# Kernel optimization log

Measured on AMD Instinct MI355X. Metric: run time of the kernel, lower is better.

Reference implementation:

```python
import jax, jax.numpy as jnp
import numpy as np

B, S, H, D = 2, 4096, 32, 128
R = 2            # num_reflectors
BASE = 10000.0   # rope base
EPS = 1e-6


def setup_inputs() -> dict:
    key = jax.random.key(0)
    k1, k2, k3 = jax.random.split(key, 3)
    q = jax.random.normal(k1, (B, S, H, D), jnp.float32)
    k = jax.random.normal(k2, (B, S, H, D), jnp.float32)
    pos = jnp.arange(S, dtype=jnp.float32)
    reflectors = jax.random.normal(k3, (H, R, D), jnp.float32)
    return {"q": q, "k": k, "pos": pos, "reflectors": reflectors}


def _apply_householder(x, reflectors, eps):
    # x: [B,S,H,D]; reflectors: [H,R,D]. Apply chain of per-head reflections
    # H = prod_r (I - 2 v_r v_r^T / (||v_r||^2 + eps)).
    n_refl = reflectors.shape[1]
    for r in range(n_refl):  # small fixed loop over reflectors
        v = reflectors[:, r, :]                      # [H,D]
        vf = v.astype(jnp.float32)
        sq = jnp.sum(vf * vf, axis=-1) + eps         # [H], fp32 accumulation
        dot = jnp.einsum('bshd,hd->bsh', x.astype(jnp.float32), vf)  # [B,S,H]
        coef = (2.0 * dot / sq).astype(x.dtype)      # [B,S,H]
        x = x - coef[..., None] * v                  # rank-1 update per head
    return x


def _rope(x, pos, base):
    # Block-diagonal 2x2 rotations on adjacent pairs (rope_ndim=2).
    d = x.shape[-1]
    d2 = d // 2
    inv_freq = base ** (-(jnp.arange(d2, dtype=jnp.float32) * 2.0) / d)  # [d2]
    ang = pos[:, None] * inv_freq                     # [S,d2]
    cos = jnp.cos(ang)[None, :, None, :]              # [1,S,1,d2]
    sin = jnp.sin(ang)[None, :, None, :]
    xr = x.reshape(*x.shape[:-1], d2, 2)              # [B,S,H,d2,2]
    x0, x1 = xr[..., 0], xr[..., 1]
    out = jnp.stack([x0 * cos - x1 * sin, x0 * sin + x1 * cos], axis=-1)
    return out.reshape(x.shape)


def reference(q, k, pos, reflectors):
    qh = _apply_householder(q, reflectors, EPS)
    kh = _apply_householder(k, reflectors, EPS)
    return _rope(qh, pos, BASE), _rope(kh, pos, BASE)
```

## Files before the change

kernel.cpp:

```cpp
#include <hip/hip_runtime.h>
#include <math.h>

#define BB 2
#define SS 4096
#define HH 32
#define DD 128
#define EPS_C 1e-6f
#define C_LOG (-0.20762050593046015f)

__device__ __forceinline__ float half_reduce(float v) {
    v += __shfl_xor(v, 1, 64);
    v += __shfl_xor(v, 2, 64);
    v += __shfl_xor(v, 4, 64);
    v += __shfl_xor(v, 8, 64);
    v += __shfl_xor(v, 16, 64);
    return v;
}

__global__ __launch_bounds__(256)
void hh_rope_kernel(const float* __restrict__ q, const float* __restrict__ k,
                    const float* __restrict__ pos, const float* __restrict__ refl,
                    float* __restrict__ oq, float* __restrict__ ok)
{
    const int lane   = threadIdx.x & 63;
    const int wid    = blockIdx.x * (blockDim.x >> 6) + (threadIdx.x >> 6);
    const int nW     = gridDim.x * (blockDim.x >> 6);
    const int hp     = wid & 15;
    const int slice  = wid >> 4;
    const int nSlice = nW >> 4;
    const int half   = lane >> 5;
    const int j      = lane & 31;
    const int h      = hp * 2 + half;

    const float4 v0 = ((const float4*)(refl + (size_t)(h * 2 + 0) * DD))[j];
    const float4 v1 = ((const float4*)(refl + (size_t)(h * 2 + 1) * DD))[j];
    const float rs0 = 2.0f / (half_reduce(v0.x*v0.x + v0.y*v0.y + v0.z*v0.z + v0.w*v0.w) + EPS_C);
    const float rs1 = 2.0f / (half_reduce(v1.x*v1.x + v1.y*v1.y + v1.z*v1.z + v1.w*v1.w) + EPS_C);

    const float if0 = exp2f((float)(2 * j)     * C_LOG);
    const float if1 = exp2f((float)(2 * j + 1) * C_LOG);

    for (int bs = slice; bs < BB * SS; bs += nSlice) {
        const float p = pos[bs & (SS - 1)];
        const size_t off = ((size_t)bs * HH + h) * DD + 4 * (size_t)j;

        float4 xq = *(const float4*)(q + off);
        float4 xk = *(const float4*)(k + off);

        float dq = half_reduce(xq.x*v0.x + xq.y*v0.y + xq.z*v0.z + xq.w*v0.w) * rs0;
        float dk = half_reduce(xk.x*v0.x + xk.y*v0.y + xk.z*v0.z + xk.w*v0.w) * rs0;
        xq.x -= dq * v0.x; xq.y -= dq * v0.y; xq.z -= dq * v0.z; xq.w -= dq * v0.w;
        xk.x -= dk * v0.x; xk.y -= dk * v0.y; xk.z -= dk * v0.z; xk.w -= dk * v0.w;

        dq = half_reduce(xq.x*v1.x + xq.y*v1.y + xq.z*v1.z + xq.w*v1.w) * rs1;
        dk = half_reduce(xk.x*v1.x + xk.y*v1.y + xk.z*v1.z + xk.w*v1.w) * rs1;
        xq.x -= dq * v1.x; xq.y -= dq * v1.y; xq.z -= dq * v1.z; xq.w -= dq * v1.w;
        xk.x -= dk * v1.x; xk.y -= dk * v1.y; xk.z -= dk * v1.z; xk.w -= dk * v1.w;

        float s0, c0, s1, c1;
        __sincosf(p * if0, &s0, &c0);
        __sincosf(p * if1, &s1, &c1);

        float4 rq, rk;
        rq.x = xq.x * c0 - xq.y * s0;  rq.y = xq.x * s0 + xq.y * c0;
        rq.z = xq.z * c1 - xq.w * s1;  rq.w = xq.z * s1 + xq.w * c1;
        rk.x = xk.x * c0 - xk.y * s0;  rk.y = xk.x * s0 + xk.y * c0;
        rk.z = xk.z * c1 - xk.w * s1;  rk.w = xk.z * s1 + xk.w * c1;

        *(float4*)(oq + off) = rq;
        *(float4*)(ok + off) = rk;
    }
}

extern "C" void kernel_launch(void* const* d_in, const int* in_sizes, int n_in,
                              void* d_out, int out_size, void* d_ws, size_t ws_size,
                              hipStream_t stream) {
    const float* q    = (const float*)d_in[0];
    const float* k    = (const float*)d_in[1];
    const float* pos  = (const float*)d_in[2];
    const float* refl = (const float*)d_in[3];

    float* oq = (float*)d_out;
    float* ok = oq + (size_t)BB * SS * HH * DD;

    hh_rope_kernel<<<dim3(2048), dim3(256), 0, stream>>>(q, k, pos, refl, oq, ok);
}
```

Measured before the change: 438.7 us.

## Fuse both Householder reflections algebraically, process two rows per iteration, nontemporal IO

```diff
diff --git a/kernel.cpp b/kernel.cpp
--- a/kernel.cpp
+++ b/kernel.cpp
@@ -8,67 +8,95 @@
 #define EPS_C 1e-6f
 #define C_LOG (-0.20762050593046015f)
 
-__device__ __forceinline__ float half_reduce(float v) {
-    v += __shfl_xor(v, 1, 64);
-    v += __shfl_xor(v, 2, 64);
-    v += __shfl_xor(v, 4, 64);
-    v += __shfl_xor(v, 8, 64);
-    v += __shfl_xor(v, 16, 64);
+typedef float vf4 __attribute__((ext_vector_type(4)));
+
+__device__ __forceinline__ float hsum32(float v) {
+    v += __int_as_float(__builtin_amdgcn_ds_swizzle(__float_as_int(v), 0x041F));
+    v += __int_as_float(__builtin_amdgcn_ds_swizzle(__float_as_int(v), 0x081F));
+    v += __int_as_float(__builtin_amdgcn_ds_swizzle(__float_as_int(v), 0x101F));
+    v += __int_as_float(__builtin_amdgcn_ds_swizzle(__float_as_int(v), 0x201F));
+    v += __int_as_float(__builtin_amdgcn_ds_swizzle(__float_as_int(v), 0x401F));
     return v;
 }
 
-__global__ __launch_bounds__(256)
+__device__ __forceinline__ float dot4(vf4 a, vf4 b) {
+    return a.x * b.x + a.y * b.y + a.z * b.z + a.w * b.w;
+}
+
+__device__ __forceinline__ vf4 finish(vf4 x, vf4 v0, vf4 v1,
+                                      float d0, float d1,
+                                      float rs0, float rs1, float t01,
+                                      float sa, float ca, float sb, float cb) {
+    const float c0 = d0 * rs0;
+    const float c1 = (d1 - c0 * t01) * rs1;
+    x.x -= c0 * v0.x + c1 * v1.x;
+    x.y -= c0 * v0.y + c1 * v1.y;
+    x.z -= c0 * v0.z + c1 * v1.z;
+    x.w -= c0 * v0.w + c1 * v1.w;
+    vf4 r;
+    r.x = x.x * ca - x.y * sa;  r.y = x.x * sa + x.y * ca;
+    r.z = x.z * cb - x.w * sb;  r.w = x.z * sb + x.w * cb;
+    return r;
+}
+
+__global__ __launch_bounds__(256, 6)
 void hh_rope_kernel(const float* __restrict__ q, const float* __restrict__ k,
                     const float* __restrict__ pos, const float* __restrict__ refl,
                     float* __restrict__ oq, float* __restrict__ ok)
 {
     const int lane   = threadIdx.x & 63;
-    const int wid    = blockIdx.x * (blockDim.x >> 6) + (threadIdx.x >> 6);
-    const int nW     = gridDim.x * (blockDim.x >> 6);
+    const int wid    = (blockIdx.x << 2) + (threadIdx.x >> 6);
     const int hp     = wid & 15;
     const int slice  = wid >> 4;
-    const int nSlice = nW >> 4;
     const int half   = lane >> 5;
     const int j      = lane & 31;
-    const int h      = hp * 2 + half;
+    const int h      = (hp << 1) + half;
 
-    const float4 v0 = ((const float4*)(refl + (size_t)(h * 2 + 0) * DD))[j];
-    const float4 v1 = ((const float4*)(refl + (size_t)(h * 2 + 1) * DD))[j];
-    const float rs0 = 2.0f / (half_reduce(v0.x*v0.x + v0.y*v0.y + v0.z*v0.z + v0.w*v0.w) + EPS_C);
-    const float rs1 = 2.0f / (half_reduce(v1.x*v1.x + v1.y*v1.y + v1.z*v1.z + v1.w*v1.w) + EPS_C);
+    const vf4 v0 = ((const vf4*)(refl + (size_t)(h * 2 + 0) * DD))[j];
+    const vf4 v1 = ((const vf4*)(refl + (size_t)(h * 2 + 1) * DD))[j];
+    const float rs0 = 2.0f / (hsum32(dot4(v0, v0)) + EPS_C);
+    const float rs1 = 2.0f / (hsum32(dot4(v1, v1)) + EPS_C);
+    const float t01 = hsum32(dot4(v1, v0));
 
     const float if0 = exp2f((float)(2 * j)     * C_LOG);
     const float if1 = exp2f((float)(2 * j + 1) * C_LOG);
 
-    for (int bs = slice; bs < BB * SS; bs += nSlice) {
-        const float p = pos[bs & (SS - 1)];
-        const size_t off = ((size_t)bs * HH + h) * DD + 4 * (size_t)j;
+    for (int bs = slice << 1; bs < BB * SS; bs += 1024) {
+        const size_t row0 = ((size_t)bs * HH + h) * DD + 4 * (size_t)j;
+        const size_t row1 = row0 + (size_t)HH * DD;
 
-        float4 xq = *(const float4*)(q + off);
-        float4 xk = *(const float4*)(k + off);
+        vf4 xq0 = __builtin_nontemporal_load((const vf4*)(q + row0));
+        vf4 xk0 = __builtin_nontemporal_load((const vf4*)(k + row0));
+        vf4 xq1 = __builtin_nontemporal_load((const vf4*)(q + row1));
+        vf4 xk1 = __builtin_nontemporal_load((const vf4*)(k + row1));
 
-        float dq = half_reduce(xq.x*v0.x + xq.y*v0.y + xq.z*v0.z + xq.w*v0.w) * rs0;
-        float dk = half_reduce(xk.x*v0.x + xk.y*v0.y + xk.z*v0.z + xk.w*v0.w) * rs0;
-        xq.x -= dq * v0.x; xq.y -= dq * v0.y; xq.z -= dq * v0.z; xq.w -= dq * v0.w;
-        xk.x -= dk * v0.x; xk.y -= dk * v0.y; xk.z -= dk * v0.z; xk.w -= dk * v0.w;
+        const float p0 = pos[bs & (SS - 1)];
+        const float p1 = pos[(bs + 1) & (SS - 1)];
 
-        dq = half_reduce(xq.x*v1.x + xq.y*v1.y + xq.z*v1.z + xq.w*v1.w) * rs1;
-        dk = half_reduce(xk.x*v1.x + xk.y*v1.y + xk.z*v1.z + xk.w*v1.w) * rs1;
-        xq.x -= dq * v1.x; xq.y -= dq * v1.y; xq.z -= dq * v1.z; xq.w -= dq * v1.w;
-        xk.x -= dk * v1.x; xk.y -= dk * v1.y; xk.z -= dk * v1.z; xk.w -= dk * v1.w;
+        float sA0, cA0, sB0, cB0, sA1, cA1, sB1, cB1;
+        __sincosf(p0 * if0, &sA0, &cA0);
+        __sincosf(p0 * if1, &sB0, &cB0);
+        __sincosf(p1 * if0, &sA1, &cA1);
+        __sincosf(p1 * if1, &sB1, &cB1);
 
-        float s0, c0, s1, c1;
-        __sincosf(p * if0, &s0, &c0);
-        __sincosf(p * if1, &s1, &c1);
+        const float dq00 = hsum32(dot4(xq0, v0));
+        const float dq01 = hsum32(dot4(xq0, v1));
+        const float dk00 = hsum32(dot4(xk0, v0));
+        const float dk01 = hsum32(dot4(xk0, v1));
+        const float dq10 = hsum32(dot4(xq1, v0));
+        const float dq11 = hsum32(dot4(xq1, v1));
+        const float dk10 = hsum32(dot4(xk1, v0));
+        const float dk11 = hsum32(dot4(xk1, v1));
 
-        float4 rq, rk;
-        rq.x = xq.x * c0 - xq.y * s0;  rq.y = xq.x * s0 + xq.y * c0;
-        rq.z = xq.z * c1 - xq.w * s1;  rq.w = xq.z * s1 + xq.w * c1;
-        rk.x = xk.x * c0 - xk.y * s0;  rk.y = xk.x * s0 + xk.y * c0;
-        rk.z = xk.z * c1 - xk.w * s1;  rk.w = xk.z * s1 + xk.w * c1;
-
-        *(float4*)(oq + off) = rq;
-        *(float4*)(ok + off) = rk;
+        vf4 r;
+        r = finish(xq0, v0, v1, dq00, dq01, rs0, rs1, t01, sA0, cA0, sB0, cB0);
+        __builtin_nontemporal_store(r, (vf4*)(oq + row0));
+        r = finish(xk0, v0, v1, dk00, dk01, rs0, rs1, t01, sA0, cA0, sB0, cB0);
+        __builtin_nontemporal_store(r, (vf4*)(ok + row0));
+        r = finish(xq1, v0, v1, dq10, dq11, rs0, rs1, t01, sA1, cA1, sB1, cB1);
+        __builtin_nontemporal_store(r, (vf4*)(oq + row1));
+        r = finish(xk1, v0, v1, dk10, dk11, rs0, rs1, t01, sA1, cA1, sB1, cB1);
+        __builtin_nontemporal_store(r, (vf4*)(ok + row1));
     }
 }
 
```

New measurement: 426.7 us. 1.03x faster.
